# Kernel optimization log

Measured on AMD Instinct MI355X. Metric: run time of the kernel, lower is better.

Reference implementation:

```python
import jax, jax.numpy as jnp
import numpy as np

B, N, D, C = 8, 400, 768, 3
K = 0.4
# Original keeps ranked positions whose argsort value (original index) < k*N.
# That count is static: M = #{j in [0,N) : j < k*N}
M = int(np.sum(np.arange(N) < K * N))  # 160
# static off-diagonal pair index lists (i != j), row-major like the nested loops
_ii, _jj = np.nonzero(~np.eye(M, dtype=bool))
II = jnp.asarray(_ii)
JJ = jnp.asarray(_jj)


def setup_inputs() -> dict:
    key = jax.random.key(0)
    k1, k2, k3, k4 = jax.random.split(key, 4)
    x = jax.random.normal(k1, (B, N, D), dtype=jnp.float32)
    w_span = jax.random.normal(k2, (D, 1), dtype=jnp.float32) * 0.02
    b_span = jnp.zeros((1,), dtype=jnp.float32)
    w_pair = jax.random.normal(k3, (3 * D, C), dtype=jnp.float32) * 0.02
    b_pair = jnp.zeros((C,), dtype=jnp.float32)
    span_ranges = jax.random.randint(k4, (N, 2), 0, 40, dtype=jnp.int32)
    return {"x": x, "w_span": w_span, "b_span": b_span,
            "w_pair": w_pair, "b_pair": b_pair, "span_ranges": span_ranges}


def reference(x, w_span, b_span, w_pair, b_pair, span_ranges):
    # span scorer: Linear(D,1) + sigmoid -> [B, N]
    h = jax.nn.sigmoid(x @ w_span + b_span)[..., 0]
    # torch.argsort(descending=True)
    order = jnp.argsort(-h, axis=-1)  # [B, N], original span indices in rank order
    # keep ranked positions j where order[b, j] < k*N (exactly M per row)
    pos = jnp.sort(jnp.where(order < K * N, jnp.arange(N), N), axis=-1)[:, :M]  # [B, M]
    # gather selected spans (built under no_grad in the original)
    x_ranked = jax.lax.stop_gradient(jnp.take_along_axis(x, pos[:, :, None], axis=1))  # [B, M, D]
    ranges_ranked = span_ranges[pos]  # [B, M, 2]

    # pair scorer decomposed over the concat [x_i, x_j, x_i*x_j]
    w1, w2, w3 = w_pair[:D], w_pair[D:2 * D], w_pair[2 * D:]
    a = x_ranked @ w1  # [B, M, C] contribution of x_i
    b = x_ranked @ w2  # [B, M, C] contribution of x_j
    mult = x_ranked[:, :, None, :] * x_ranked[:, None, :, :]  # [B, M, M, D]
    logits = a[:, :, None, :] + b[:, None, :, :] + mult @ w3 + b_pair  # [B, M, M, C]
    probs = jax.nn.softmax(jax.nn.sigmoid(logits), axis=-1)

    pair_probs = probs[:, II, JJ]  # [B, M*(M-1), C], off-diagonal pairs
    pair_ranges = jnp.stack([ranges_ranked[:, II], ranges_ranked[:, JJ]], axis=2)  # [B, P, 2, 2]
    return pair_probs, pair_ranges
```

## Files before the change

kernel.cpp:

```cpp
#include <hip/hip_runtime.h>
#include <math.h>

constexpr int B_ = 8;
constexpr int N_ = 400;
constexpr int D_ = 768;
constexpr int M_ = 160;
constexpr int PAIRS_ = M_ * (M_ - 1);

typedef __attribute__((ext_vector_type(8))) short short8;
typedef __attribute__((ext_vector_type(4))) float floatx4;


__global__ __launch_bounds__(256) void k_span(const float* __restrict__ x,
                                              const float* __restrict__ w_span,
                                              double* __restrict__ z) {
  int wg = blockIdx.x * 4 + (threadIdx.x >> 6);
  int lane = threadIdx.x & 63;
  const float* xr = x + (size_t)wg * D_;
  double acc = 0.0;
#pragma unroll
  for (int k = 0; k < D_ / 64; ++k) {
    int d = lane + (k << 6);
    acc += (double)xr[d] * (double)w_span[d];
  }
#pragma unroll
  for (int off = 32; off > 0; off >>= 1)
    acc += __shfl_down(acc, off, 64);
  if (lane == 0) z[wg] = acc;
}

__global__ __launch_bounds__(256) void k_rank(const double* __restrict__ z,
                                              int* __restrict__ pos) {
  __shared__ double zsh[N_];
  __shared__ int ranksh[M_];
  int b = blockIdx.x;
  int t = threadIdx.x;
  for (int j = t; j < N_; j += 256) zsh[j] = z[b * N_ + j];
  __syncthreads();
  if (t < M_) {
    double zi = zsh[t];
    int cnt = 0;
    for (int j = 0; j < N_; ++j) {
      double zj = zsh[j];
      cnt += (zj > zi) || (zj == zi && j < t);
    }
    ranksh[t] = cnt;
  }
  __syncthreads();
  if (t < M_) {
    int r = ranksh[t];
    int slot = 0;
#pragma unroll 8
    for (int k = 0; k < M_; ++k) slot += (ranksh[k] < r);
    pos[b * M_ + slot] = r;
  }
}

__global__ __launch_bounds__(256) void k_ab(const float* __restrict__ x,
                                            const float* __restrict__ w_pair,
                                            const float* __restrict__ b_pair,
                                            const int* __restrict__ pos,
                                            float* __restrict__ aterm,
                                            float* __restrict__ bterm) {
  int wg = blockIdx.x * 4 + (threadIdx.x >> 6);
  int lane = threadIdx.x & 63;
  int b = wg / M_;
  int row = pos[wg];
  const float* xr = x + ((size_t)(b * N_ + row)) * D_;
  float a0 = 0, a1 = 0, a2 = 0, c0 = 0, c1 = 0, c2 = 0;
#pragma unroll 4
  for (int k = 0; k < D_ / 64; ++k) {
    int d = lane + (k << 6);
    float xv = xr[d];
    a0 += xv * w_pair[d * 3 + 0];
    a1 += xv * w_pair[d * 3 + 1];
    a2 += xv * w_pair[d * 3 + 2];
    c0 += xv * w_pair[(D_ + d) * 3 + 0];
    c1 += xv * w_pair[(D_ + d) * 3 + 1];
    c2 += xv * w_pair[(D_ + d) * 3 + 2];
  }
#pragma unroll
  for (int off = 32; off > 0; off >>= 1) {
    a0 += __shfl_down(a0, off, 64);
    a1 += __shfl_down(a1, off, 64);
    a2 += __shfl_down(a2, off, 64);
    c0 += __shfl_down(c0, off, 64);
    c1 += __shfl_down(c1, off, 64);
    c2 += __shfl_down(c2, off, 64);
  }
  if (lane == 0) {
    aterm[wg * 3 + 0] = a0 + b_pair[0];
    aterm[wg * 3 + 1] = a1 + b_pair[1];
    aterm[wg * 3 + 2] = a2 + b_pair[2];
    bterm[wg * 3 + 0] = c0;
    bterm[wg * 3 + 1] = c1;
    bterm[wg * 3 + 2] = c2;
  }
}

__device__ inline void split8(const float* v, short8* hi, short8* lo) {
  short8 h, l;
#pragma unroll
  for (int e = 0; e < 8; ++e) {
    float f = v[e];
    unsigned int hb = __float_as_uint(f) & 0xffff0000u;
    h[e] = (short)(hb >> 16);
    float rest = f - __uint_as_float(hb);
    l[e] = (short)(__float_as_uint(rest) >> 16);
  }
  *hi = h;
  *lo = l;
}

__global__ __launch_bounds__(256) void k_pairs(const float* __restrict__ x,
                                               const float* __restrict__ w_pair,
                                               const int* __restrict__ pos,
                                               const float* __restrict__ aterm,
                                               const float* __restrict__ bterm,
                                               const int* __restrict__ span_ranges,
                                               float* __restrict__ out_probs,
                                               float4* __restrict__ out_ranges) {
  int lane = threadIdx.x & 63;
  int w = blockIdx.x * 4 + (threadIdx.x >> 6);
  int b = w / 100;
  int t = w - b * 100;
  int ti = t / 10;
  int tj = t - ti * 10;
  int quad = lane >> 4;
  int l16 = lane & 15;

  int i_lane = ti * 16 + l16;
  int j_lane = tj * 16 + l16;
  int pa = pos[b * M_ + i_lane];
  int pb = pos[b * M_ + j_lane];
  const float* xa = x + ((size_t)(b * N_ + pa)) * D_ + quad * 8;
  const float* xb = x + ((size_t)(b * N_ + pb)) * D_ + quad * 8;
  const float* w3 = w_pair + 2 * D_ * 3;

  floatx4 acc0 = {0.f, 0.f, 0.f, 0.f};
  floatx4 acc1 = {0.f, 0.f, 0.f, 0.f};
  floatx4 acc2 = {0.f, 0.f, 0.f, 0.f};

  for (int k = 0; k < D_; k += 32) {
    float xaf[8], xbf[8], wv[24];
    *(float4*)(xaf + 0) = *(const float4*)(xa + k + 0);
    *(float4*)(xaf + 4) = *(const float4*)(xa + k + 4);
    *(float4*)(xbf + 0) = *(const float4*)(xb + k + 0);
    *(float4*)(xbf + 4) = *(const float4*)(xb + k + 4);
    int d0 = k + quad * 8;
    const float* wp = w3 + (size_t)d0 * 3;
#pragma unroll
    for (int q = 0; q < 6; ++q) *(float4*)(wv + 4 * q) = *(const float4*)(wp + 4 * q);

    short8 bhi, blo;
    split8(xbf, &bhi, &blo);

#pragma unroll
    for (int c = 0; c < 3; ++c) {
      float y[8];
#pragma unroll
      for (int e = 0; e < 8; ++e) y[e] = xaf[e] * wv[e * 3 + c];
      short8 ahi, alo;
      split8(y, &ahi, &alo);
      floatx4 acc = (c == 0) ? acc0 : (c == 1) ? acc1 : acc2;
      acc = __builtin_amdgcn_mfma_f32_16x16x32_bf16(ahi, bhi, acc, 0, 0, 0);
      acc = __builtin_amdgcn_mfma_f32_16x16x32_bf16(ahi, blo, acc, 0, 0, 0);
      acc = __builtin_amdgcn_mfma_f32_16x16x32_bf16(alo, bhi, acc, 0, 0, 0);
      if (c == 0) acc0 = acc; else if (c == 1) acc1 = acc; else acc2 = acc;
    }
  }

  const float* at = aterm + (size_t)b * M_ * 3;
  const float* bt = bterm + (size_t)b * M_ * 3;
  int j = j_lane;
  float bj0 = bt[j * 3 + 0], bj1 = bt[j * 3 + 1], bj2 = bt[j * 3 + 2];
  int rj0 = span_ranges[pb * 2 + 0], rj1 = span_ranges[pb * 2 + 1];

#pragma unroll
  for (int r = 0; r < 4; ++r) {
    int i = ti * 16 + quad * 4 + r;
    if (i == j) continue;
    float l0 = acc0[r] + at[i * 3 + 0] + bj0;
    float l1 = acc1[r] + at[i * 3 + 1] + bj1;
    float l2 = acc2[r] + at[i * 3 + 2] + bj2;
    float s0 = 1.0f / (1.0f + expf(-l0));
    float s1 = 1.0f / (1.0f + expf(-l1));
    float s2 = 1.0f / (1.0f + expf(-l2));
    float e0 = expf(s0), e1 = expf(s1), e2 = expf(s2);
    float inv = 1.0f / (e0 + e1 + e2);
    int jj = j - (j > i ? 1 : 0);
    size_t p = (size_t)b * PAIRS_ + (size_t)i * (M_ - 1) + jj;
    out_probs[p * 3 + 0] = e0 * inv;
    out_probs[p * 3 + 1] = e1 * inv;
    out_probs[p * 3 + 2] = e2 * inv;
    int pi = pos[b * M_ + i];
    float4 rg;
    rg.x = (float)span_ranges[pi * 2 + 0];
    rg.y = (float)span_ranges[pi * 2 + 1];
    rg.z = (float)rj0;
    rg.w = (float)rj1;
    out_ranges[p] = rg;
  }
}

extern "C" void kernel_launch(void* const* d_in, const int* in_sizes, int n_in,
                              void* d_out, int out_size, void* d_ws, size_t ws_size,
                              hipStream_t stream) {
  const float* x = (const float*)d_in[0];
  const float* w_span = (const float*)d_in[1];
  const float* w_pair = (const float*)d_in[3];
  const float* b_pair = (const float*)d_in[4];
  const int* span_ranges = (const int*)d_in[5];

  char* ws = (char*)d_ws;
  double* z = (double*)ws;
  int* pos = (int*)(ws + 25600);
  float* aterm = (float*)(ws + 30720);
  float* bterm = (float*)(ws + 46080);

  float* out = (float*)d_out;
  float* out_probs = out;
  float4* out_ranges = (float4*)(out + (size_t)B_ * PAIRS_ * 3);

  k_span<<<(B_ * N_) / 4, 256, 0, stream>>>(x, w_span, z);
  k_rank<<<B_, 256, 0, stream>>>(z, pos);
  k_ab<<<(B_ * M_) / 4, 256, 0, stream>>>(x, w_pair, b_pair, pos, aterm, bterm);
  k_pairs<<<(B_ * 100) / 4, 256, 0, stream>>>(x, w_pair, pos, aterm, bterm,
                                              span_ranges, out_probs, out_ranges);
}
```

Baseline: 109.2 us.

## Precompute bf16 hi/lo splits in span pass and fuse rank with a/b terms

The span-score kernel now also writes bf16 hi/lo splits of x and of x*w3 for each of the three classes, for all N rows. The pair kernel then loads these pre-split operands directly instead of re-splitting floats on every tile. Ranking and the a/b projection are merged into one kernel with 8 blocks, removing one launch. The trade-off is about 39MB of extra workspace writes for all 400 rows, not just the 160 selected ones, plus a low-parallelism a/b stage.

Result: slower. 181.0 us (+65.8%).

```diff
diff --git a/kernel.cpp b/kernel.cpp
--- a/kernel.cpp
+++ b/kernel.cpp
@@ -6,33 +6,58 @@
 constexpr int D_ = 768;
 constexpr int M_ = 160;
 constexpr int PAIRS_ = M_ * (M_ - 1);
+constexpr size_t BND_ = (size_t)B_ * N_ * D_;
 
 typedef __attribute__((ext_vector_type(8))) short short8;
 typedef __attribute__((ext_vector_type(4))) float floatx4;
 
 
-__global__ __launch_bounds__(256) void k_span(const float* __restrict__ x,
+__global__ __launch_bounds__(256) void k_prep(const float* __restrict__ x,
                                               const float* __restrict__ w_span,
-                                              double* __restrict__ z) {
-  int wg = blockIdx.x * 4 + (threadIdx.x >> 6);
+                                              const float* __restrict__ w_pair,
+                                              double* __restrict__ z,
+                                              short* __restrict__ Xh,
+                                              short* __restrict__ Xl,
+                                              short* __restrict__ Yh,
+                                              short* __restrict__ Yl) {
+  int row = blockIdx.x * 4 + (threadIdx.x >> 6);
   int lane = threadIdx.x & 63;
-  const float* xr = x + (size_t)wg * D_;
+  const float* xr = x + (size_t)row * D_;
+  const float* w3 = w_pair + 2 * D_ * 3;
   double acc = 0.0;
 #pragma unroll
   for (int k = 0; k < D_ / 64; ++k) {
     int d = lane + (k << 6);
-    acc += (double)xr[d] * (double)w_span[d];
+    float f = xr[d];
+    acc += (double)f * (double)w_span[d];
+    size_t o = (size_t)row * D_ + d;
+    unsigned hb = __float_as_uint(f) & 0xffff0000u;
+    Xh[o] = (short)(hb >> 16);
+    Xl[o] = (short)(__float_as_uint(f - __uint_as_float(hb)) >> 16);
+#pragma unroll
+    for (int c = 0; c < 3; ++c) {
+      float y = f * w3[d * 3 + c];
+      unsigned yh = __float_as_uint(y) & 0xffff0000u;
+      Yh[(size_t)c * BND_ + o] = (short)(yh >> 16);
+      Yl[(size_t)c * BND_ + o] = (short)(__float_as_uint(y - __uint_as_float(yh)) >> 16);
+    }
   }
 #pragma unroll
   for (int off = 32; off > 0; off >>= 1)
     acc += __shfl_down(acc, off, 64);
-  if (lane == 0) z[wg] = acc;
-}
-
-__global__ __launch_bounds__(256) void k_rank(const double* __restrict__ z,
-                                              int* __restrict__ pos) {
+  if (lane == 0) z[row] = acc;
+}
+
+__global__ __launch_bounds__(256) void k_rank_ab(const double* __restrict__ z,
+                                                 const float* __restrict__ x,
+                                                 const float* __restrict__ w_pair,
+                                                 const float* __restrict__ b_pair,
+                                                 int* __restrict__ pos,
+                                                 float* __restrict__ aterm,
+                                                 float* __restrict__ bterm) {
   __shared__ double zsh[N_];
   __shared__ int ranksh[M_];
+  __shared__ int possh[M_];
   int b = blockIdx.x;
   int t = threadIdx.x;
   for (int j = t; j < N_; j += 256) zsh[j] = z[b * N_ + j];
@@ -52,68 +77,52 @@
     int slot = 0;
 #pragma unroll 8
     for (int k = 0; k < M_; ++k) slot += (ranksh[k] < r);
+    possh[slot] = r;
     pos[b * M_ + slot] = r;
   }
-}
-
-__global__ __launch_bounds__(256) void k_ab(const float* __restrict__ x,
-                                            const float* __restrict__ w_pair,
-                                            const float* __restrict__ b_pair,
-                                            const int* __restrict__ pos,
-                                            float* __restrict__ aterm,
-                                            float* __restrict__ bterm) {
-  int wg = blockIdx.x * 4 + (threadIdx.x >> 6);
-  int lane = threadIdx.x & 63;
-  int b = wg / M_;
-  int row = pos[wg];
-  const float* xr = x + ((size_t)(b * N_ + row)) * D_;
-  float a0 = 0, a1 = 0, a2 = 0, c0 = 0, c1 = 0, c2 = 0;
+  __syncthreads();
+
+  int wave = t >> 6, lane = t & 63;
+  for (int i = wave; i < M_; i += 4) {
+    int row = possh[i];
+    const float* xr = x + ((size_t)(b * N_ + row)) * D_;
+    float a0 = 0, a1 = 0, a2 = 0, c0 = 0, c1 = 0, c2 = 0;
 #pragma unroll 4
-  for (int k = 0; k < D_ / 64; ++k) {
-    int d = lane + (k << 6);
-    float xv = xr[d];
-    a0 += xv * w_pair[d * 3 + 0];
-    a1 += xv * w_pair[d * 3 + 1];
-    a2 += xv * w_pair[d * 3 + 2];
-    c0 += xv * w_pair[(D_ + d) * 3 + 0];
-    c1 += xv * w_pair[(D_ + d) * 3 + 1];
-    c2 += xv * w_pair[(D_ + d) * 3 + 2];
-  }
-#pragma unroll
-  for (int off = 32; off > 0; off >>= 1) {
-    a0 += __shfl_down(a0, off, 64);
-    a1 += __shfl_down(a1, off, 64);
-    a2 += __shfl_down(a2, off, 64);
-    c0 += __shfl_down(c0, off, 64);
-    c1 += __shfl_down(c1, off, 64);
-    c2 += __shfl_down(c2, off, 64);
-  }
-  if (lane == 0) {
-    aterm[wg * 3 + 0] = a0 + b_pair[0];
-    aterm[wg * 3 + 1] = a1 + b_pair[1];
-    aterm[wg * 3 + 2] = a2 + b_pair[2];
-    bterm[wg * 3 + 0] = c0;
-    bterm[wg * 3 + 1] = c1;
-    bterm[wg * 3 + 2] = c2;
-  }
-}
-
-__device__ inline void split8(const float* v, short8* hi, short8* lo) {
-  short8 h, l;
-#pragma unroll
-  for (int e = 0; e < 8; ++e) {
-    float f = v[e];
-    unsigned int hb = __float_as_uint(f) & 0xffff0000u;
-    h[e] = (short)(hb >> 16);
-    float rest = f - __uint_as_float(hb);
-    l[e] = (short)(__float_as_uint(rest) >> 16);
-  }
-  *hi = h;
-  *lo = l;
-}
-
-__global__ __launch_bounds__(256) void k_pairs(const float* __restrict__ x,
-                                               const float* __restrict__ w_pair,
+    for (int k = 0; k < D_ / 64; ++k) {
+      int d = lane + (k << 6);
+      float xv = xr[d];
+      a0 += xv * w_pair[d * 3 + 0];
+      a1 += xv * w_pair[d * 3 + 1];
+      a2 += xv * w_pair[d * 3 + 2];
+      c0 += xv * w_pair[(D_ + d) * 3 + 0];
+      c1 += xv * w_pair[(D_ + d) * 3 + 1];
+      c2 += xv * w_pair[(D_ + d) * 3 + 2];
+    }
+#pragma unroll
+    for (int off = 32; off > 0; off >>= 1) {
+      a0 += __shfl_down(a0, off, 64);
+      a1 += __shfl_down(a1, off, 64);
+      a2 += __shfl_down(a2, off, 64);
+      c0 += __shfl_down(c0, off, 64);
+      c1 += __shfl_down(c1, off, 64);
+      c2 += __shfl_down(c2, off, 64);
+    }
+    if (lane == 0) {
+      int wg = b * M_ + i;
+      aterm[wg * 3 + 0] = a0 + b_pair[0];
+      aterm[wg * 3 + 1] = a1 + b_pair[1];
+      aterm[wg * 3 + 2] = a2 + b_pair[2];
+      bterm[wg * 3 + 0] = c0;
+      bterm[wg * 3 + 1] = c1;
+      bterm[wg * 3 + 2] = c2;
+    }
+  }
+}
+
+__global__ __launch_bounds__(256) void k_pairs(const short* __restrict__ Xh,
+                                               const short* __restrict__ Xl,
+                                               const short* __restrict__ Yh,
+                                               const short* __restrict__ Yl,
                                                const int* __restrict__ pos,
                                                const float* __restrict__ aterm,
                                                const float* __restrict__ bterm,
@@ -133,41 +142,42 @@
   int j_lane = tj * 16 + l16;
   int pa = pos[b * M_ + i_lane];
   int pb = pos[b * M_ + j_lane];
-  const float* xa = x + ((size_t)(b * N_ + pa)) * D_ + quad * 8;
-  const float* xb = x + ((size_t)(b * N_ + pb)) * D_ + quad * 8;
-  const float* w3 = w_pair + 2 * D_ * 3;
+  size_t oa = ((size_t)(b * N_ + pa)) * D_ + quad * 8;
+  size_t ob = ((size_t)(b * N_ + pb)) * D_ + quad * 8;
+
+  const short* ah0 = Yh + 0 * BND_ + oa;
+  const short* ah1 = Yh + 1 * BND_ + oa;
+  const short* ah2 = Yh + 2 * BND_ + oa;
+  const short* al0 = Yl + 0 * BND_ + oa;
+  const short* al1 = Yl + 1 * BND_ + oa;
+  const short* al2 = Yl + 2 * BND_ + oa;
+  const short* bhp = Xh + ob;
+  const short* blp = Xl + ob;
 
   floatx4 acc0 = {0.f, 0.f, 0.f, 0.f};
   floatx4 acc1 = {0.f, 0.f, 0.f, 0.f};
   floatx4 acc2 = {0.f, 0.f, 0.f, 0.f};
 
+#pragma unroll 4
   for (int k = 0; k < D_; k += 32) {
-    float xaf[8], xbf[8], wv[24];
-    *(float4*)(xaf + 0) = *(const float4*)(xa + k + 0);
-    *(float4*)(xaf + 4) = *(const float4*)(xa + k + 4);
-    *(float4*)(xbf + 0) = *(const float4*)(xb + k + 0);
-    *(float4*)(xbf + 4) = *(const float4*)(xb + k + 4);
-    int d0 = k + quad * 8;
-    const float* wp = w3 + (size_t)d0 * 3;
-#pragma unroll
-    for (int q = 0; q < 6; ++q) *(float4*)(wv + 4 * q) = *(const float4*)(wp + 4 * q);
-
-    short8 bhi, blo;
-    split8(xbf, &bhi, &blo);
-
-#pragma unroll
-    for (int c = 0; c < 3; ++c) {
-      float y[8];
-#pragma unroll
-      for (int e = 0; e < 8; ++e) y[e] = xaf[e] * wv[e * 3 + c];
-      short8 ahi, alo;
-      split8(y, &ahi, &alo);
-      floatx4 acc = (c == 0) ? acc0 : (c == 1) ? acc1 : acc2;
-      acc = __builtin_amdgcn_mfma_f32_16x16x32_bf16(ahi, bhi, acc, 0, 0, 0);
-      acc = __builtin_amdgcn_mfma_f32_16x16x32_bf16(ahi, blo, acc, 0, 0, 0);
-      acc = __builtin_amdgcn_mfma_f32_16x16x32_bf16(alo, bhi, acc, 0, 0, 0);
-      if (c == 0) acc0 = acc; else if (c == 1) acc1 = acc; else acc2 = acc;
-    }
+    short8 bh = *(const short8*)(bhp + k);
+    short8 bl = *(const short8*)(blp + k);
+    short8 h0 = *(const short8*)(ah0 + k);
+    short8 l0 = *(const short8*)(al0 + k);
+    short8 h1 = *(const short8*)(ah1 + k);
+    short8 l1 = *(const short8*)(al1 + k);
+    short8 h2 = *(const short8*)(ah2 + k);
+    short8 l2 = *(const short8*)(al2 + k);
+
+    acc0 = __builtin_amdgcn_mfma_f32_16x16x32_bf16(h0, bh, acc0, 0, 0, 0);
+    acc0 = __builtin_amdgcn_mfma_f32_16x16x32_bf16(h0, bl, acc0, 0, 0, 0);
+    acc0 = __builtin_amdgcn_mfma_f32_16x16x32_bf16(l0, bh, acc0, 0, 0, 0);
+    acc1 = __builtin_amdgcn_mfma_f32_16x16x32_bf16(h1, bh, acc1, 0, 0, 0);
+    acc1 = __builtin_amdgcn_mfma_f32_16x16x32_bf16(h1, bl, acc1, 0, 0, 0);
+    acc1 = __builtin_amdgcn_mfma_f32_16x16x32_bf16(l1, bh, acc1, 0, 0, 0);
+    acc2 = __builtin_amdgcn_mfma_f32_16x16x32_bf16(h2, bh, acc2, 0, 0, 0);
+    acc2 = __builtin_amdgcn_mfma_f32_16x16x32_bf16(h2, bl, acc2, 0, 0, 0);
+    acc2 = __builtin_amdgcn_mfma_f32_16x16x32_bf16(l2, bh, acc2, 0, 0, 0);
   }
 
   const float* at = aterm + (size_t)b * M_ * 3;
@@ -217,14 +227,17 @@
   int* pos = (int*)(ws + 25600);
   float* aterm = (float*)(ws + 30720);
   float* bterm = (float*)(ws + 46080);
+  short* Xh = (short*)(ws + 61440);
+  short* Xl = (short*)(ws + 4976640);
+  short* Yh = (short*)(ws + 9891840);
+  short* Yl = (short*)(ws + 24637440);
 
   float* out = (float*)d_out;
   float* out_probs = out;
   float4* out_ranges = (float4*)(out + (size_t)B_ * PAIRS_ * 3);
 
-  k_span<<<(B_ * N_) / 4, 256, 0, stream>>>(x, w_span, z);
-  k_rank<<<B_, 256, 0, stream>>>(z, pos);
-  k_ab<<<(B_ * M_) / 4, 256, 0, stream>>>(x, w_pair, b_pair, pos, aterm, bterm);
-  k_pairs<<<(B_ * 100) / 4, 256, 0, stream>>>(x, w_pair, pos, aterm, bterm,
+  k_prep<<<(B_ * N_) / 4, 256, 0, stream>>>(x, w_span, w_pair, z, Xh, Xl, Yh, Yl);
+  k_rank_ab<<<B_, 256, 0, stream>>>(z, x, w_pair, b_pair, pos, aterm, bterm);
+  k_pairs<<<(B_ * 100) / 4, 256, 0, stream>>>(Xh, Xl, Yh, Yl, pos, aterm, bterm,
                                               span_ranges, out_probs, out_ranges);
 }
```
